# Kernel optimization log

Hardware: AMD Instinct MI355X
Metric: run time of the kernel (lower is better)

The kernel has to match this reference:

```python
import jax, jax.numpy as jnp
import numpy as np

B, N, D, H = 8, 1024, 256, 8
HD = D // H  # head_dim = 32
EPS = 1e-06


def setup_inputs() -> dict:
    key = jax.random.key(0)
    ks = jax.random.split(key, 8)
    x = jax.random.normal(ks[0], (B, N, D), dtype=jnp.float32)
    adj = jax.random.randint(ks[1], (B, N, N), 0, 2, dtype=jnp.int32)
    # Parameters
    W_w = jax.random.normal(ks[2], (D, D), dtype=jnp.float32) / np.sqrt(D)
    W_b = jnp.zeros((D,), dtype=jnp.float32)
    # a: xavier_uniform over [num_heads, 2*head_dim]
    lim = np.sqrt(6.0 / (H + 2 * HD))
    a = jax.random.uniform(ks[3], (H, 2 * HD), minval=-lim, maxval=lim, dtype=jnp.float32)
    gamma = jnp.ones((D,), dtype=jnp.float32)
    beta = jnp.zeros((D,), dtype=jnp.float32)
    return {"x": x, "adj": adj, "W_w": W_w, "W_b": W_b, "a": a, "gamma": gamma, "beta": beta}


def reference(x, adj, W_w, W_b, a, gamma, beta):
    residual = x
    h = jnp.einsum('bnd,od->bno', x, W_w) + W_b          # [B,N,D]
    h = h.reshape(B, N, H, HD).transpose(0, 2, 1, 3)     # [B,H,N,hd]
    # Faithful to original einsum 'bnijh,bh->bnij': `a` is indexed by the
    # BATCH axis (requires batch==num_heads). Decompose concat-dot into two
    # O(N) projections summed pairwise (same math, no O(N^2) concat tensor).
    s_i = jnp.einsum('bhnd,bd->bhn', h, a[:, :HD])       # [B,H,N]
    s_j = jnp.einsum('bhnd,bd->bhn', h, a[:, HD:])       # [B,H,N]
    scores = s_i[:, :, :, None] + s_j[:, :, None, :]     # [B,H,N,N]
    scores = jnp.where(scores >= 0, scores, 0.2 * scores)  # LeakyReLU(0.2)
    mask = (1.0 - adj.astype(scores.dtype))[:, None] * -1e9
    attn = jax.nn.softmax(scores + mask, axis=-1)        # [B,H,N,N]
    out = jnp.einsum('bhij,bhjd->bhid', attn, h)         # [B,H,N,hd]
    out = out.transpose(0, 2, 1, 3).reshape(B, N, D)
    out = out + residual
    # LayerNorm with torch unbiased std, divide by (std + eps)
    mean = out.mean(axis=-1, keepdims=True)
    var = ((out - mean) ** 2).mean(axis=-1, keepdims=True) * (D / (D - 1))
    out = (out - mean) / (jnp.sqrt(var) + EPS)
    return out * gamma + beta
```

## Files before the change

kernel.cpp:

```cpp
#include <hip/hip_runtime.h>
#include <hip/hip_bf16.h>
#include <math.h>

#define Bq 8
#define Nq 1024
#define Dq 256
#define Hq 8
#define HDq 32
#define LOG2E 1.44269504f

typedef __attribute__((ext_vector_type(8)))  short short8v;
typedef __attribute__((ext_vector_type(4)))  float f32x4;
typedef __attribute__((ext_vector_type(16))) float f32x16;

__device__ __forceinline__ void gload_lds16(const void* g, void* l) {
    __builtin_amdgcn_global_load_lds(
        (const __attribute__((address_space(1))) void*)g,
        (__attribute__((address_space(3))) void*)l, 16, 0, 0);
}

__global__ __launch_bounds__(256) void gemm_pack(const float* __restrict__ x,
                                                 const float* __restrict__ W,
                                                 const float* __restrict__ Wb,
                                                 const float* __restrict__ a,
                                                 const int* __restrict__ adj,
                                                 __hip_bfloat16* __restrict__ h_bT,
                                                 float* __restrict__ s_i2,
                                                 float* __restrict__ s_j2,
                                                 unsigned* __restrict__ adjw) {
    __shared__ __hip_bfloat16 xs[64][68];
    __shared__ __hip_bfloat16 wsm[64][68];
    __shared__ __hip_bfloat16 ht[64][72];
    const int t = threadIdx.x;
    const int lane = t & 63, wv = t >> 6;

    if (blockIdx.x >= 512) {
        const size_t row = ((size_t)blockIdx.x - 512) * 4 + wv;
        const int* ar = adj + row * Nq;
        unsigned* wr = adjw + row * 32;
        #pragma unroll
        for (int it = 0; it < 16; ++it) {
            int v = ar[it * 64 + lane];
            unsigned long long mask = __ballot(v != 0);
            if (lane == 0) {
                wr[it * 2 + 0] = (unsigned)mask;
                wr[it * 2 + 1] = (unsigned)(mask >> 32);
            }
        }
        return;
    }

    const int m0 = (blockIdx.x & 127) * 64;
    const int o0 = (blockIdx.x >> 7) * 64;
    const int lo = lane & 31, hi = lane >> 5;
    const int mw = (wv & 1) * 32, ow = (wv >> 1) * 32;
    const int b = m0 >> 10;
    f32x16 acc = 0.f;

    for (int k0 = 0; k0 < 256; k0 += 64) {
        __syncthreads();
        #pragma unroll
        for (int it = 0; it < 4; ++it) {
            int f4  = t + it * 256;
            int row = f4 >> 4;
            int c4  = (f4 & 15) * 4;
            float4 xv = *(const float4*)(x + (size_t)(m0 + row) * 256 + k0 + c4);
            float4 wv2 = *(const float4*)(W + (size_t)(o0 + row) * 256 + k0 + c4);
            union { ushort4 u; __bf16 e[4]; } xb, wb;
            xb.e[0] = (__bf16)xv.x; xb.e[1] = (__bf16)xv.y;
            xb.e[2] = (__bf16)xv.z; xb.e[3] = (__bf16)xv.w;
            wb.e[0] = (__bf16)wv2.x; wb.e[1] = (__bf16)wv2.y;
            wb.e[2] = (__bf16)wv2.z; wb.e[3] = (__bf16)wv2.w;
            *(ushort4*)(&xs[row][c4])  = xb.u;
            *(ushort4*)(&wsm[row][c4]) = wb.u;
        }
        __syncthreads();
        #pragma unroll
        for (int kk = 0; kk < 4; ++kk) {
            short8v av = *(const short8v*)(&xs[mw + lo][kk * 16 + hi * 8]);
            short8v bv = *(const short8v*)(&wsm[ow + lo][kk * 16 + hi * 8]);
            acc = __builtin_amdgcn_mfma_f32_32x32x16_bf16(av, bv, acc, 0, 0, 0);
        }
    }

    __syncthreads();
    const float bias = Wb[o0 + ow + lo];
    #pragma unroll
    for (int rg = 0; rg < 16; ++rg) {
        int row = (rg & 3) + 8 * (rg >> 2) + 4 * hi;
        float v = acc[rg] + bias;
        ht[ow + lo][mw + row] = (__hip_bfloat16)v;
    }
    __syncthreads();

    #pragma unroll
    for (int it = 0; it < 2; ++it) {
        int s8 = t + it * 256;
        int ol = s8 >> 3;
        int n8 = (s8 & 7) * 8;
        short8v v = *(const short8v*)(&ht[ol][n8]);
        int o = o0 + ol;
        size_t drow = (size_t)((b * Hq + (o >> 5)) * HDq + (o & 31));
        *(short8v*)((unsigned short*)h_bT + drow * Nq + (m0 & 1023) + n8) = v;
    }
    {
        int which = t >> 7;
        int hd = (t >> 6) & 1, nl = t & 63;
        const float* ab = a + b * 64 + which * 32;
        float s = 0.f;
        #pragma unroll
        for (int d = 0; d < 32; ++d)
            s += (float)ht[hd * 32 + d][nl] * ab[d];
        int bh = b * Hq + (o0 >> 5) + hd;
        int n  = (m0 & 1023) + nl;
        (which ? s_j2 : s_i2)[(size_t)bh * Nq + n] = s * LOG2E;
    }
}

__global__ __launch_bounds__(256, 4) void attn_v9(const __hip_bfloat16* __restrict__ h_bT,
                                                  const unsigned* __restrict__ adjw,
                                                  const float* __restrict__ s_i2,
                                                  const float* __restrict__ s_j2,
                                                  __hip_bfloat16* __restrict__ att) {
    __shared__ __hip_bfloat16 hsT[2][32][256];
    __shared__ float sjs[2][256];
    const int t = threadIdx.x, lane = t & 63, wv = t >> 6;
    const int id = ((int)blockIdx.x & 7) * 128 + ((int)blockIdx.x >> 3);
    const int bh = id >> 4;
    const int b  = bh >> 3, hh = bh & 7;
    const int i0 = (id & 15) * 64 + wv * 16;
    const int r16 = lane & 15, jg = lane >> 4;
    const int iG = i0 + r16;
    const int key = r16 & 7;
    const unsigned shbase = jg * 8;

    const float si = s_i2[(size_t)bh * Nq + iG];
    const unsigned short* hb = (const unsigned short*)h_bT + (size_t)bh * HDq * Nq;
    const float* sjb = s_j2 + (size_t)bh * Nq;
    const unsigned* awp = adjw + ((size_t)b * Nq + iG) * 32;

    auto stage = [&](int nb, int ch) {
        #pragma unroll
        for (int it = 0; it < 4; ++it) {
            int rrb = wv * 8 + it * 2;
            int rr  = rrb + (lane >> 5);
            int oct = (lane & 31) ^ (rr & 7);
            const unsigned short* src = hb + (size_t)rr * Nq + ch * 256 + (oct << 3);
            gload_lds16(src, &hsT[nb][rrb][0]);
        }
        gload_lds16(sjb + ch * 256 + lane * 4, &sjs[nb][0]);
    };

    short8v ones;
    #pragma unroll
    for (int k = 0; k < 8; ++k) ones[k] = (short)0x3F80;

    f32x4 acc0 = 0.f, acc1 = 0.f, accl = 0.f;
    uint4 qa[2], qb[2];

    stage(0, 0);
    qa[0] = *(const uint4*)(awp);
    qb[0] = *(const uint4*)(awp + 4);

    #pragma unroll
    for (int c = 0; c < 4; ++c) {
        const int cb = c & 1;
        if (c < 3) {
            stage(cb ^ 1, c + 1);
            qa[cb ^ 1] = *(const uint4*)(awp + (c + 1) * 8);
            qb[cb ^ 1] = *(const uint4*)(awp + (c + 1) * 8 + 4);
        }
        if (c < 3) asm volatile("s_waitcnt vmcnt(7)" ::: "memory");
        else       asm volatile("s_waitcnt vmcnt(0)" ::: "memory");
        __builtin_amdgcn_s_barrier();
        __builtin_amdgcn_sched_barrier(0);

        unsigned aw8[8] = {qa[cb].x, qa[cb].y, qa[cb].z, qa[cb].w,
                           qb[cb].x, qb[cb].y, qb[cb].z, qb[cb].w};
        const __hip_bfloat16* pr0 = &hsT[cb][r16][0];
        const __hip_bfloat16* pr1 = &hsT[cb][r16 + 16][0];

        #pragma unroll
        for (int w = 0; w < 8; ++w) {
            unsigned wbits = aw8[w] >> shbase;
            int po = ((w * 4 + jg) ^ key) << 3;
            short8v fb0 = *(const short8v*)(pr0 + po);
            short8v fb1 = *(const short8v*)(pr1 + po);
            f32x4 sv0 = *(const f32x4*)(&sjs[cb][w * 32 + jg * 8]);
            f32x4 sv1 = *(const f32x4*)(&sjs[cb][w * 32 + jg * 8 + 4]);
            union { short8v v; __bf16 e[8]; } pa;
            #pragma unroll
            for (int e = 0; e < 8; ++e) {
                float sc = si + (e < 4 ? sv0[e] : sv1[e - 4]);
                sc = fmaxf(sc, 0.2f * sc);
                sc = ((wbits >> e) & 1u) ? sc : -30000.f;
                pa.e[e] = (__bf16)__builtin_amdgcn_exp2f(sc);
            }
            acc0 = __builtin_amdgcn_mfma_f32_16x16x32_bf16(pa.v, fb0, acc0, 0, 0, 0);
            acc1 = __builtin_amdgcn_mfma_f32_16x16x32_bf16(pa.v, fb1, acc1, 0, 0, 0);
            accl = __builtin_amdgcn_mfma_f32_16x16x32_bf16(pa.v, ones, accl, 0, 0, 0);
        }
        asm volatile("s_waitcnt lgkmcnt(0)" ::: "memory");
        __builtin_amdgcn_s_barrier();
    }

    #pragma unroll
    for (int rg = 0; rg < 4; ++rg) {
        int row = jg * 4 + rg;
        float rl = 1.f / accl[rg];
        size_t base = ((size_t)b * Nq + i0 + row) * Dq + hh * HDq;
        att[base + r16]      = (__hip_bfloat16)(acc0[rg] * rl);
        att[base + 16 + r16] = (__hip_bfloat16)(acc1[rg] * rl);
    }
}

__global__ __launch_bounds__(256) void ln_k(const __hip_bfloat16* __restrict__ att,
                                            const float* __restrict__ x,
                                            const float* __restrict__ gamma,
                                            const float* __restrict__ beta,
                                            float* __restrict__ out) {
    const int t = threadIdx.x, lane = t & 63, wv = t >> 6;
    const size_t row  = (size_t)blockIdx.x * 4 + wv;
    const size_t base = row * Dq + lane * 4;
    union { ushort4 u; __hip_bfloat16 e[4]; } av;
    av.u = *(const ushort4*)((const unsigned short*)att + base);
    float4 xv = *(const float4*)(x + base);
    float o0 = (float)av.e[0] + xv.x, o1 = (float)av.e[1] + xv.y;
    float o2 = (float)av.e[2] + xv.z, o3 = (float)av.e[3] + xv.w;
    float s  = o0 + o1 + o2 + o3;
    float sq = o0 * o0 + o1 * o1 + o2 * o2 + o3 * o3;
    #pragma unroll
    for (int off = 32; off; off >>= 1) {
        s  += __shfl_xor(s, off);
        sq += __shfl_xor(sq, off);
    }
    float mean = s * (1.f / 256.f);
    float var  = (sq - 256.f * mean * mean) * (1.f / 255.f);
    var = fmaxf(var, 0.f);
    float inv = 1.f / (sqrtf(var) + 1e-6f);
    float4 g  = *(const float4*)(gamma + lane * 4);
    float4 bt = *(const float4*)(beta + lane * 4);
    float4 ov;
    ov.x = (o0 - mean) * inv * g.x + bt.x;
    ov.y = (o1 - mean) * inv * g.y + bt.y;
    ov.z = (o2 - mean) * inv * g.z + bt.z;
    ov.w = (o3 - mean) * inv * g.w + bt.w;
    *(float4*)(out + base) = ov;
}

extern "C" void kernel_launch(void* const* d_in, const int* in_sizes, int n_in,
                              void* d_out, int out_size, void* d_ws, size_t ws_size,
                              hipStream_t stream) {
    const float* x     = (const float*)d_in[0];
    const int*   adj   = (const int*)d_in[1];
    const float* W_w   = (const float*)d_in[2];
    const float* W_b   = (const float*)d_in[3];
    const float* a     = (const float*)d_in[4];
    const float* gamma = (const float*)d_in[5];
    const float* beta  = (const float*)d_in[6];
    float* out = (float*)d_out;

    __hip_bfloat16* h_bT = (__hip_bfloat16*)d_ws;
    __hip_bfloat16* att  = (__hip_bfloat16*)((char*)d_ws + (size_t)Bq * Hq * Nq * HDq * 2);
    float* s_i2 = (float*)((char*)att + (size_t)Bq * Nq * Dq * 2);
    float* s_j2 = s_i2 + (size_t)Bq * Hq * Nq;
    unsigned* adjw = (unsigned*)(s_j2 + (size_t)Bq * Hq * Nq);

    gemm_pack<<<2560, 256, 0, stream>>>(x, W_w, W_b, a, adj, h_bT, s_i2, s_j2, adjw);
    attn_v9<<<1024, 256, 0, stream>>>(h_bT, adjw, s_i2, s_j2, att);
    ln_k<<<2048, 256, 0, stream>>>(att, x, gamma, beta, out);
}
```

Measured before the change: 45.08 us.

## Split key chunks across waves and reduce partial attention outputs in LDS

Each wave used to own 16 query rows and walk all keys in every staged chunk. Now each wave takes all 64 query rows of the block but only a quarter of each key chunk. Partial numerators and denominators are combined through shared memory at the end, which is then written out with vectorized stores. This reuses each LDS B-fragment across four query groups, cutting LDS reads per MFMA. The cost is more accumulator registers, a final cross-wave reduction with an extra barrier, and shared memory reused for that reduction.

```diff
diff --git a/kernel.cpp b/kernel.cpp
--- a/kernel.cpp
+++ b/kernel.cpp
@@ -117,27 +117,34 @@
     }
 }
 
-__global__ __launch_bounds__(256, 4) void attn_v9(const __hip_bfloat16* __restrict__ h_bT,
-                                                  const unsigned* __restrict__ adjw,
-                                                  const float* __restrict__ s_i2,
-                                                  const float* __restrict__ s_j2,
-                                                  __hip_bfloat16* __restrict__ att) {
-    __shared__ __hip_bfloat16 hsT[2][32][256];
-    __shared__ float sjs[2][256];
+__global__ __launch_bounds__(256, 4) void attn_v10(const __hip_bfloat16* __restrict__ h_bT,
+                                                   const unsigned* __restrict__ adjw,
+                                                   const float* __restrict__ s_i2,
+                                                   const float* __restrict__ s_j2,
+                                                   __hip_bfloat16* __restrict__ att) {
+    __shared__ char smem[36352];
+    auto hsT = (unsigned short (*)[32][256])smem;
+    auto sjs = (float (*)[256])(smem + 32768);
+    auto comb  = (float (*)[32][69])smem;
+    float* combl = (float*)(smem + 35328);
+
     const int t = threadIdx.x, lane = t & 63, wv = t >> 6;
     const int id = ((int)blockIdx.x & 7) * 128 + ((int)blockIdx.x >> 3);
     const int bh = id >> 4;
     const int b  = bh >> 3, hh = bh & 7;
-    const int i0 = (id & 15) * 64 + wv * 16;
+    const int i0 = (id & 15) * 64;
     const int r16 = lane & 15, jg = lane >> 4;
-    const int iG = i0 + r16;
     const int key = r16 & 7;
     const unsigned shbase = jg * 8;
 
-    const float si = s_i2[(size_t)bh * Nq + iG];
+    float si[4];
+    #pragma unroll
+    for (int it = 0; it < 4; ++it)
+        si[it] = s_i2[(size_t)bh * Nq + i0 + it * 16 + r16];
+
     const unsigned short* hb = (const unsigned short*)h_bT + (size_t)bh * HDq * Nq;
     const float* sjb = s_j2 + (size_t)bh * Nq;
-    const unsigned* awp = adjw + ((size_t)b * Nq + iG) * 32;
+    const unsigned* aw0 = adjw + ((size_t)b * Nq + i0 + r16) * 32 + wv * 2;
 
     auto stage = [&](int nb, int ch) {
         #pragma unroll
@@ -145,72 +152,88 @@
             int rrb = wv * 8 + it * 2;
             int rr  = rrb + (lane >> 5);
             int oct = (lane & 31) ^ (rr & 7);
-            const unsigned short* src = hb + (size_t)rr * Nq + ch * 256 + (oct << 3);
-            gload_lds16(src, &hsT[nb][rrb][0]);
+            gload_lds16(hb + (size_t)rr * Nq + ch * 256 + (oct << 3),
+                        &hsT[nb][rrb][0]);
         }
         gload_lds16(sjb + ch * 256 + lane * 4, &sjs[nb][0]);
     };
 
+    uint2 qm[2][4];
+    auto loadmasks = [&](int nb, int ch) {
+        #pragma unroll
+        for (int it = 0; it < 4; ++it)
+            qm[nb][it] = *(const uint2*)(aw0 + ch * 8 + it * 512);
+    };
+
     short8v ones;
     #pragma unroll
     for (int k = 0; k < 8; ++k) ones[k] = (short)0x3F80;
 
-    f32x4 acc0 = 0.f, acc1 = 0.f, accl = 0.f;
-    uint4 qa[2], qb[2];
+    f32x4 acc[4][2] = {};
+    f32x4 accl4[4] = {};
 
     stage(0, 0);
-    qa[0] = *(const uint4*)(awp);
-    qb[0] = *(const uint4*)(awp + 4);
+    loadmasks(0, 0);
 
     #pragma unroll
     for (int c = 0; c < 4; ++c) {
         const int cb = c & 1;
-        if (c < 3) {
-            stage(cb ^ 1, c + 1);
-            qa[cb ^ 1] = *(const uint4*)(awp + (c + 1) * 8);
-            qb[cb ^ 1] = *(const uint4*)(awp + (c + 1) * 8 + 4);
-        }
-        if (c < 3) asm volatile("s_waitcnt vmcnt(7)" ::: "memory");
+        if (c < 3) { stage(cb ^ 1, c + 1); loadmasks(cb ^ 1, c + 1); }
+        if (c < 3) asm volatile("s_waitcnt vmcnt(9)" ::: "memory");
         else       asm volatile("s_waitcnt vmcnt(0)" ::: "memory");
         __builtin_amdgcn_s_barrier();
         __builtin_amdgcn_sched_barrier(0);
 
-        unsigned aw8[8] = {qa[cb].x, qa[cb].y, qa[cb].z, qa[cb].w,
-                           qb[cb].x, qb[cb].y, qb[cb].z, qb[cb].w};
-        const __hip_bfloat16* pr0 = &hsT[cb][r16][0];
-        const __hip_bfloat16* pr1 = &hsT[cb][r16 + 16][0];
-
-        #pragma unroll
-        for (int w = 0; w < 8; ++w) {
-            unsigned wbits = aw8[w] >> shbase;
-            int po = ((w * 4 + jg) ^ key) << 3;
-            short8v fb0 = *(const short8v*)(pr0 + po);
-            short8v fb1 = *(const short8v*)(pr1 + po);
-            f32x4 sv0 = *(const f32x4*)(&sjs[cb][w * 32 + jg * 8]);
-            f32x4 sv1 = *(const f32x4*)(&sjs[cb][w * 32 + jg * 8 + 4]);
-            union { short8v v; __bf16 e[8]; } pa;
+        #pragma unroll
+        for (int w = 0; w < 2; ++w) {
+            int oct = (wv * 8 + w * 4 + jg) ^ key;
+            short8v fb0 = *(const short8v*)(&hsT[cb][r16][oct << 3]);
+            short8v fb1 = *(const short8v*)(&hsT[cb][r16 + 16][oct << 3]);
+            f32x4 sv0 = *(const f32x4*)(&sjs[cb][wv * 64 + w * 32 + jg * 8]);
+            f32x4 sv1 = *(const f32x4*)(&sjs[cb][wv * 64 + w * 32 + jg * 8 + 4]);
             #pragma unroll
-            for (int e = 0; e < 8; ++e) {
-                float sc = si + (e < 4 ? sv0[e] : sv1[e - 4]);
-                sc = fmaxf(sc, 0.2f * sc);
-                sc = ((wbits >> e) & 1u) ? sc : -30000.f;
-                pa.e[e] = (__bf16)__builtin_amdgcn_exp2f(sc);
+            for (int it = 0; it < 4; ++it) {
+                unsigned wbits = (w ? qm[cb][it].y : qm[cb][it].x) >> shbase;
+                union { short8v v; __bf16 e[8]; } pa;
+                #pragma unroll
+                for (int e = 0; e < 8; ++e) {
+                    float sc = si[it] + (e < 4 ? sv0[e] : sv1[e - 4]);
+                    sc = fmaxf(sc, 0.2f * sc);
+                    sc = ((wbits >> e) & 1u) ? sc : -30000.f;
+                    pa.e[e] = (__bf16)__builtin_amdgcn_exp2f(sc);
+                }
+                acc[it][0] = __builtin_amdgcn_mfma_f32_16x16x32_bf16(pa.v, fb0, acc[it][0], 0, 0, 0);
+                acc[it][1] = __builtin_amdgcn_mfma_f32_16x16x32_bf16(pa.v, fb1, acc[it][1], 0, 0, 0);
+                accl4[it]  = __builtin_amdgcn_mfma_f32_16x16x32_bf16(pa.v, ones, accl4[it], 0, 0, 0);
             }
-            acc0 = __builtin_amdgcn_mfma_f32_16x16x32_bf16(pa.v, fb0, acc0, 0, 0, 0);
-            acc1 = __builtin_amdgcn_mfma_f32_16x16x32_bf16(pa.v, fb1, acc1, 0, 0, 0);
-            accl = __builtin_amdgcn_mfma_f32_16x16x32_bf16(pa.v, ones, accl, 0, 0, 0);
         }
         asm volatile("s_waitcnt lgkmcnt(0)" ::: "memory");
         __builtin_amdgcn_s_barrier();
     }
 
     #pragma unroll
-    for (int rg = 0; rg < 4; ++rg) {
-        int row = jg * 4 + rg;
-        float rl = 1.f / accl[rg];
-        size_t base = ((size_t)b * Nq + i0 + row) * Dq + hh * HDq;
-        att[base + r16]      = (__hip_bfloat16)(acc0[rg] * rl);
-        att[base + 16 + r16] = (__hip_bfloat16)(acc1[rg] * rl);
+    for (int it = 0; it < 4; ++it) {
+        *(f32x4*)(&comb[wv][r16][it * 16 + jg * 4])      = acc[it][0];
+        *(f32x4*)(&comb[wv][r16 + 16][it * 16 + jg * 4]) = acc[it][1];
+        if (r16 == 0)
+            *(f32x4*)(&combl[wv * 64 + it * 16 + jg * 4]) = accl4[it];
+    }
+    __syncthreads();
+
+    {
+        const int i  = t >> 2;
+        const int dq = t & 3;
+        float l = combl[i] + combl[64 + i] + combl[128 + i] + combl[192 + i];
+        float rl = 1.f / l;
+        union { short8v v; __hip_bfloat16 e[8]; } ov;
+        #pragma unroll
+        for (int k = 0; k < 8; ++k) {
+            int d = dq * 8 + k;
+            float s = comb[0][d][i] + comb[1][d][i] + comb[2][d][i] + comb[3][d][i];
+            ov.e[k] = (__hip_bfloat16)(s * rl);
+        }
+        *(short8v*)((unsigned short*)att + ((size_t)b * Nq + i0 + i) * Dq
+                    + hh * HDq + dq * 8) = ov.v;
     }
 }
 
@@ -267,6 +290,6 @@
     unsigned* adjw = (unsigned*)(s_j2 + (size_t)Bq * Hq * Nq);
 
     gemm_pack<<<2560, 256, 0, stream>>>(x, W_w, W_b, a, adj, h_bT, s_i2, s_j2, adjw);
-    attn_v9<<<1024, 256, 0, stream>>>(h_bT, adjw, s_i2, s_j2, att);
+    attn_v10<<<1024, 256, 0, stream>>>(h_bT, adjw, s_i2, s_j2, att);
     ln_k<<<2048, 256, 0, stream>>>(att, x, gamma, beta, out);
 }
```

Measured after the change: 50.16 us. +11.3%, slower.
